# Kernel optimization log

Measured on AMD Instinct MI355X. Metric: run time of the kernel, lower is better.

Reference implementation:

```python
import jax, jax.numpy as jnp
import numpy as np
import math

B, T, EMB, HD = 4, 2048, 2048, 128
HALF = HD // 2


def setup_inputs() -> dict:
    key = jax.random.key(0)
    ks = jax.random.split(key, 4)
    x = jax.random.normal(ks[0], (B, T, EMB), dtype=jnp.float32)
    s = 1.0 / math.sqrt(EMB)
    Wq = jax.random.normal(ks[1], (EMB, HD), dtype=jnp.float32) * s
    Wk = jax.random.normal(ks[2], (EMB, HD), dtype=jnp.float32) * s
    Wv = jax.random.normal(ks[3], (EMB, HD), dtype=jnp.float32) * s
    # Standard RoPE rotation table: theta_i = 10000^(-2i/HD), angle = pos * theta
    inv_freq = 1.0 / (10000.0 ** (np.arange(0, HALF, dtype=np.float32) / HALF))
    angles = np.arange(T, dtype=np.float32)[:, None] * inv_freq[None, :]  # [T, HALF]
    rot_cos = jnp.asarray(np.cos(angles), dtype=jnp.float32)
    rot_sin = jnp.asarray(np.sin(angles), dtype=jnp.float32)
    # Additive causal mask: 0 on/below diagonal, -1e9 above
    NEG = -1e9
    mask = jnp.where(jnp.tril(jnp.ones((T, T), dtype=bool)), 0.0, NEG).astype(jnp.float32)
    return {"x": x, "Wq": Wq, "Wk": Wk, "Wv": Wv,
            "rot_cos": rot_cos, "rot_sin": rot_sin, "mask": mask}


def _apply_rope(q, rot_cos, rot_sin):
    # q: [B, T, HD]; view last dim as HALF complex pairs and rotate
    qp = q.reshape(q.shape[0], q.shape[1], HALF, 2)
    re, im = qp[..., 0], qp[..., 1]
    out_re = re * rot_cos - im * rot_sin  # broadcast [T,HALF] over batch
    out_im = re * rot_sin + im * rot_cos
    return jnp.stack([out_re, out_im], axis=-1).reshape(q.shape)


def reference(x, Wq, Wk, Wv, rot_cos, rot_sin, mask):
    Q = x @ Wq  # [B, T, HD]
    K = x @ Wk
    V = x @ Wv
    Q = _apply_rope(Q, rot_cos, rot_sin)
    K = _apply_rope(K, rot_cos, rot_sin)
    scores = jnp.einsum('bqd,bkd->bqk', Q, K) / math.sqrt(HD)
    probs = jax.nn.softmax(scores + mask, axis=-1)  # dropout is identity in eval
    return jnp.einsum('bqk,bkd->bqd', probs, V)
```

## Files before the change

kernel.cpp:

```cpp
#include <hip/hip_runtime.h>
#include <cstddef>
#include <cstdint>

#define T_SEQ 2048
#define EMB_D 2048
#define HD_D  128

typedef __attribute__((ext_vector_type(8))) short short8;
typedef __attribute__((ext_vector_type(4))) float f32x4;
typedef __attribute__((ext_vector_type(4))) unsigned short ushort4v;
typedef __attribute__((ext_vector_type(8))) unsigned short ushort8v;

union frag_u { short8 s8; unsigned u[4]; };

static __device__ __forceinline__ unsigned short f2bf_rne(float f) {
    union { float f; unsigned u; } v; v.f = f;
    unsigned r = v.u + 0x7fffu + ((v.u >> 16) & 1u);
    return (unsigned short)(r >> 16);
}
static __device__ __forceinline__ unsigned short f2bf_fast(float f) {
    union { float f; unsigned u; } v; v.f = f;
    return (unsigned short)((v.u + 0x8000u) >> 16);
}
static __device__ __forceinline__ unsigned pk2(float a, float b) {
    union { float f; unsigned u; } x, y; x.f = a; y.f = b;
    return __builtin_amdgcn_perm(y.u + 0x8000u, x.u + 0x8000u, 0x07060302);
}
static __device__ __forceinline__ void dma16(const void* g, void* l) {
    __builtin_amdgcn_global_load_lds(
        (const __attribute__((address_space(1))) unsigned int*)g,
        (__attribute__((address_space(3))) unsigned int*)l, 16, 0, 0);
}
#define EXP2F(x) __builtin_amdgcn_exp2f(x)

__global__ __launch_bounds__(256) void prep_weights(
    const float* __restrict__ Wq, const float* __restrict__ Wk,
    const float* __restrict__ Wv, unsigned short* __restrict__ Wt)
{
    __shared__ __attribute__((aligned(16))) unsigned short tw[64 * 132];
    const int w = blockIdx.y;
    const int k0 = blockIdx.x * 64;
    const float* W = (w == 0) ? Wq : (w == 1) ? Wk : Wv;
    const int tid = threadIdx.x;
#pragma unroll
    for (int p = 0; p < 8; p++) {
        const int f = p * 256 + tid;
        const int row = f >> 5, c4 = f & 31;
        const float4 v = *(const float4*)&W[(size_t)(k0 + row) * HD_D + c4 * 4];
        ushort4v h = { f2bf_rne(v.x), f2bf_rne(v.y), f2bf_rne(v.z), f2bf_rne(v.w) };
        *(ushort4v*)&tw[row * 132 + c4 * 4] = h;
    }
    __syncthreads();
    const int n = tid >> 1, h = tid & 1;
    unsigned short* dst = Wt + (size_t)w * (HD_D * EMB_D) + (size_t)n * EMB_D + k0 + h * 32;
#pragma unroll
    for (int j = 0; j < 4; j++) {
        ushort8v o;
#pragma unroll
        for (int jj = 0; jj < 8; jj++) o[jj] = tw[(h * 32 + j * 8 + jj) * 132 + n];
        *(ushort8v*)&dst[j * 8] = o;
    }
}

__global__ __launch_bounds__(256, 2) void qkv_fused(
    const float* __restrict__ x, const unsigned short* __restrict__ Wt,
    const float* __restrict__ rcos, const float* __restrict__ rsin,
    unsigned short* __restrict__ Qb, unsigned short* __restrict__ Kb,
    unsigned short* __restrict__ Vt)
{
    __shared__ __attribute__((aligned(16))) float xs[2][64 * 64];
    __shared__ __attribute__((aligned(16))) unsigned short wsb[2][96 * 64];
    const int ng = blockIdx.x;
    const int m0 = blockIdx.y * 64;
    const int tid = threadIdx.x;
    const int lane = tid & 63, wave = tid >> 6;
    const int wm = wave >> 1, wn = wave & 1;
    const int l15 = lane & 15, lq = lane >> 4;

    const float* xSrc[4]; int xOff[4];
#pragma unroll
    for (int p = 0; p < 4; p++) {
        const int g = p * 256 + tid;
        const int row = g >> 4, c = g & 15;
        xSrc[p] = x + (size_t)(m0 + row) * EMB_D + (c ^ (row & 15)) * 4;
        xOff[p] = (p * 256 + wave * 64) * 4;
    }
    const unsigned short* wSrc[3]; int wOff[3];
#pragma unroll
    for (int p = 0; p < 3; p++) {
        const int g = p * 256 + tid;
        const int row = g >> 3, c = g & 7;
        wSrc[p] = Wt + (size_t)(ng * 96 + row) * EMB_D + (c ^ (row & 7)) * 8;
        wOff[p] = (p * 256 + wave * 64) * 8;
    }

    int offA[2][2][2];
#pragma unroll
    for (int i = 0; i < 2; i++)
#pragma unroll
        for (int ks = 0; ks < 2; ks++) {
            const int row = wm * 32 + i * 16 + l15;
            const int ga = ks * 8 + lq * 2;
            offA[i][ks][0] = row * 64 + ((ga)     ^ (row & 15)) * 4;
            offA[i][ks][1] = row * 64 + ((ga + 1) ^ (row & 15)) * 4;
        }
    int offB[3][2];
#pragma unroll
    for (int j = 0; j < 3; j++)
#pragma unroll
        for (int ks = 0; ks < 2; ks++) {
            const int row = wn * 48 + j * 16 + l15;
            const int gb = ks * 4 + lq;
            offB[j][ks] = row * 64 + (gb ^ (row & 7)) * 8;
        }

    f32x4 acc[2][3];
#pragma unroll
    for (int i = 0; i < 2; i++)
#pragma unroll
        for (int j = 0; j < 3; j++) acc[i][j] = (f32x4){0.f, 0.f, 0.f, 0.f};

#pragma unroll
    for (int p = 0; p < 4; p++) dma16(xSrc[p], &xs[0][xOff[p]]);
#pragma unroll
    for (int p = 0; p < 3; p++) dma16(wSrc[p], &wsb[0][wOff[p]]);

    for (int k0 = 0; k0 < EMB_D; k0 += 64) {
        const int buf = (k0 >> 6) & 1;
        __syncthreads();
        if (k0 + 64 < EMB_D) {
#pragma unroll
            for (int p = 0; p < 4; p++)
                dma16(xSrc[p] + k0 + 64, &xs[buf ^ 1][xOff[p]]);
#pragma unroll
            for (int p = 0; p < 3; p++)
                dma16(wSrc[p] + k0 + 64, &wsb[buf ^ 1][wOff[p]]);
        }

        frag_u A[2][2];
#pragma unroll
        for (int i = 0; i < 2; i++)
#pragma unroll
            for (int ks = 0; ks < 2; ks++) {
                const f32x4 f0 = *(const f32x4*)&xs[buf][offA[i][ks][0]];
                const f32x4 f1 = *(const f32x4*)&xs[buf][offA[i][ks][1]];
                A[i][ks].u[0] = pk2(f0.x, f0.y);
                A[i][ks].u[1] = pk2(f0.z, f0.w);
                A[i][ks].u[2] = pk2(f1.x, f1.y);
                A[i][ks].u[3] = pk2(f1.z, f1.w);
            }
#pragma unroll
        for (int ks = 0; ks < 2; ks++)
#pragma unroll
            for (int j = 0; j < 3; j++) {
                const short8 B = *(const short8*)&wsb[buf][offB[j][ks]];
#pragma unroll
                for (int i = 0; i < 2; i++)
                    acc[i][j] = __builtin_amdgcn_mfma_f32_16x16x32_bf16(
                        A[i][ks].s8, B, acc[i][j], 0, 0, 0);
            }
    }

    const float qscale = 0.08838834764831845f * 1.4426950408889634f;
#pragma unroll
    for (int i = 0; i < 2; i++) {
#pragma unroll
        for (int r = 0; r < 4; r++) {
            const int row = m0 + wm * 32 + i * 16 + lq * 4 + r;
            const int t = row & (T_SEQ - 1);
            const int bb = row >> 11;
#pragma unroll
            for (int j = 0; j < 3; j++) {
                const int col = ng * 96 + wn * 48 + j * 16 + l15;
                const int mat = col >> 7, mcol = col & 127;
                const float v = acc[i][j][r];
                if (mat == 2) {
                    Vt[((size_t)bb * HD_D + mcol) * T_SEQ + t] = f2bf_rne(v);
                } else {
                    const int ip = mcol >> 1;
                    const float c = rcos[t * 64 + ip];
                    const float s = rsin[t * 64 + ip];
                    const float pv = __shfl_xor(v, 1);
                    float rv = (mcol & 1) ? (pv * s + v * c) : (v * c - pv * s);
                    if (mat == 0) {
                        rv *= qscale;
                        Qb[(size_t)row * HD_D + mcol] = f2bf_rne(rv);
                    } else {
                        Kb[(size_t)row * HD_D + mcol] = f2bf_rne(rv);
                    }
                }
            }
        }
    }
}

__global__ __launch_bounds__(256, 2) void attn(
    const unsigned short* __restrict__ Qb, const unsigned short* __restrict__ Kb,
    const unsigned short* __restrict__ Vt, float* __restrict__ out)
{
    __shared__ float O_s[4][16 * 128];
    __shared__ __attribute__((aligned(16))) unsigned short P_s[4][2][16 * 40];
    __shared__ float l_s[4][16];

    const int tid = threadIdx.x;
    const int lane = tid & 63, wave = tid >> 6;
    const int l15 = lane & 15, lq = lane >> 4;
    const int kf = lq * 8;

    const int b  = blockIdx.x & 3;
    const int q0 = (127 - (blockIdx.x >> 2)) * 16;
    const int kend = q0 + 16;
    const float M2 = 16.0f;

    const unsigned short* Qp = Qb + (size_t)(b * T_SEQ + q0) * HD_D;
    short8 aQ[4];
#pragma unroll
    for (int d = 0; d < 4; d++)
        aQ[d] = *(const short8*)&Qp[l15 * HD_D + d * 32 + kf];

    f32x4 acc[8];
#pragma unroll
    for (int d = 0; d < 8; d++) acc[d] = (f32x4){0.f, 0.f, 0.f, 0.f};
    float l_r[4] = {0.f, 0.f, 0.f, 0.f};

    const unsigned short* Kbase = Kb + (size_t)b * T_SEQ * HD_D;
    const unsigned short* Vbase = Vt + (size_t)b * HD_D * T_SEQ;
    unsigned short* PwA = &P_s[wave][0][0];
    unsigned short* PwB = &P_s[wave][1][0];

    for (int c = wave; c * 32 < kend; c += 8) {
        const int kA = c * 32;
        const int kB = (c + 4) * 32;
        const bool hB = kB < kend;

        const unsigned short* KpA = Kbase + (size_t)kA * HD_D;
        const unsigned short* KpB = Kbase + (size_t)kB * HD_D;
        short8 KA[8], KB_[8];
#pragma unroll
        for (int d = 0; d < 4; d++)
#pragma unroll
            for (int n = 0; n < 2; n++)
                KA[d * 2 + n] = *(const short8*)&KpA[(size_t)(n * 16 + l15) * HD_D + d * 32 + kf];
        if (hB) {
#pragma unroll
            for (int d = 0; d < 4; d++)
#pragma unroll
                for (int n = 0; n < 2; n++)
                    KB_[d * 2 + n] = *(const short8*)&KpB[(size_t)(n * 16 + l15) * HD_D + d * 32 + kf];
        }

        f32x4 sA0 = (f32x4){0.f, 0.f, 0.f, 0.f}, sA1 = sA0, sB0 = sA0, sB1 = sA0;
#pragma unroll
        for (int d = 0; d < 4; d++) {
            sA0 = __builtin_amdgcn_mfma_f32_16x16x32_bf16(aQ[d], KA[d * 2 + 0], sA0, 0, 0, 0);
            sA1 = __builtin_amdgcn_mfma_f32_16x16x32_bf16(aQ[d], KA[d * 2 + 1], sA1, 0, 0, 0);
        }
        if (hB) {
#pragma unroll
            for (int d = 0; d < 4; d++) {
                sB0 = __builtin_amdgcn_mfma_f32_16x16x32_bf16(aQ[d], KB_[d * 2 + 0], sB0, 0, 0, 0);
                sB1 = __builtin_amdgcn_mfma_f32_16x16x32_bf16(aQ[d], KB_[d * 2 + 1], sB1, 0, 0, 0);
            }
        }

        short8 VA[8];
#pragma unroll
        for (int d = 0; d < 8; d++)
            VA[d] = *(const short8*)&Vbase[(size_t)(d * 16 + l15) * T_SEQ + kA + kf];

#pragma unroll
        for (int r = 0; r < 4; r++) {
            const int q = q0 + lq * 4 + r;
            const float p0 = ((kA + l15)      <= q) ? EXP2F(sA0[r] - M2) : 0.f;
            const float p1 = ((kA + 16 + l15) <= q) ? EXP2F(sA1[r] - M2) : 0.f;
            l_r[r] += p0 + p1;
            const int prow = (lq * 4 + r) * 40;
            PwA[prow + l15]      = f2bf_fast(p0);
            PwA[prow + 16 + l15] = f2bf_fast(p1);
        }
        const short8 pA = *(const short8*)&PwA[l15 * 40 + kf];
#pragma unroll
        for (int d = 0; d < 8; d++)
            acc[d] = __builtin_amdgcn_mfma_f32_16x16x32_bf16(pA, VA[d], acc[d], 0, 0, 0);

        if (hB) {
            short8 VB[8];
#pragma unroll
            for (int d = 0; d < 8; d++)
                VB[d] = *(const short8*)&Vbase[(size_t)(d * 16 + l15) * T_SEQ + kB + kf];
#pragma unroll
            for (int r = 0; r < 4; r++) {
                const int q = q0 + lq * 4 + r;
                const float p0 = ((kB + l15)      <= q) ? EXP2F(sB0[r] - M2) : 0.f;
                const float p1 = ((kB + 16 + l15) <= q) ? EXP2F(sB1[r] - M2) : 0.f;
                l_r[r] += p0 + p1;
                const int prow = (lq * 4 + r) * 40;
                PwB[prow + l15]      = f2bf_fast(p0);
                PwB[prow + 16 + l15] = f2bf_fast(p1);
            }
            const short8 pB = *(const short8*)&PwB[l15 * 40 + kf];
#pragma unroll
            for (int d = 0; d < 8; d++)
                acc[d] = __builtin_amdgcn_mfma_f32_16x16x32_bf16(pB, VB[d], acc[d], 0, 0, 0);
        }
    }

#pragma unroll
    for (int r = 0; r < 4; r++) {
        float lr = l_r[r];
        lr += __shfl_xor(lr, 1);
        lr += __shfl_xor(lr, 2);
        lr += __shfl_xor(lr, 4);
        lr += __shfl_xor(lr, 8);
        if (l15 == 0) l_s[wave][lq * 4 + r] = lr;
#pragma unroll
        for (int d = 0; d < 8; d++)
            O_s[wave][(lq * 4 + r) * 128 + d * 16 + l15] = acc[d][r];
    }
    __syncthreads();

    const int row = tid >> 4;
    const int dc = (tid & 15) * 8;
    const float lt = l_s[0][row] + l_s[1][row] + l_s[2][row] + l_s[3][row];
    const float inv = 1.0f / lt;
    f32x4 o0 = (f32x4){0.f, 0.f, 0.f, 0.f};
    f32x4 o1 = (f32x4){0.f, 0.f, 0.f, 0.f};
#pragma unroll
    for (int w2 = 0; w2 < 4; w2++) {
        const float* p = &O_s[w2][row * 128 + dc];
        o0 += *(const f32x4*)p;
        o1 += *(const f32x4*)(p + 4);
    }
    float* op = out + (size_t)(b * T_SEQ + q0 + row) * HD_D + dc;
    *(f32x4*)op       = o0 * inv;
    *(f32x4*)(op + 4) = o1 * inv;
}

extern "C" void kernel_launch(void* const* d_in, const int* in_sizes, int n_in,
                              void* d_out, int out_size, void* d_ws, size_t ws_size,
                              hipStream_t stream)
{
    (void)in_sizes; (void)n_in; (void)out_size; (void)ws_size;
    const float* x  = (const float*)d_in[0];
    const float* Wq = (const float*)d_in[1];
    const float* Wk = (const float*)d_in[2];
    const float* Wv = (const float*)d_in[3];
    const float* rc = (const float*)d_in[4];
    const float* rs = (const float*)d_in[5];
    float* out = (float*)d_out;

    char* ws = (char*)d_ws;
    unsigned short* Wt = (unsigned short*)(ws);
    unsigned short* Qb = (unsigned short*)(ws + 1572864);
    unsigned short* Kb = (unsigned short*)(ws + 1572864 + 2097152);
    unsigned short* Vt = (unsigned short*)(ws + 1572864 + 2 * 2097152);

    prep_weights<<<dim3(32, 3),  256, 0, stream>>>(Wq, Wk, Wv, Wt);
    qkv_fused   <<<dim3(4, 128), 256, 0, stream>>>(x, Wt, rc, rs, Qb, Kb, Vt);
    attn        <<<dim3(512),    256, 0, stream>>>(Qb, Kb, Vt, out);
}
```

Measured before the change: 199.5 us.

## Split attention KV range across two blocks and merge partials; remap QKV blocks per XCD

Each query tile's KV loop is now split across two blocks (g=0/1). Block 0 writes fp32 partial output to out and block 1 writes a bf16 partial to workspace, and a new merge kernel sums the two and divides by the combined row sums. This doubles the attention grid to fill more CUs and raises occupancy to 4 blocks per SM, with the partial-sum staging in LDS cut to bf16. The QKV GEMM grid is flattened and remapped so that consecutive row tiles land on the same XCD for L2 reuse. The cost is an extra kernel launch, an extra pass over the output, and added bf16 rounding error in the partial sums.

```diff
diff --git a/kernel.cpp b/kernel.cpp
--- a/kernel.cpp
+++ b/kernel.cpp
@@ -21,6 +21,10 @@
 static __device__ __forceinline__ unsigned short f2bf_fast(float f) {
     union { float f; unsigned u; } v; v.f = f;
     return (unsigned short)((v.u + 0x8000u) >> 16);
+}
+static __device__ __forceinline__ float bf2f(unsigned short h) {
+    union { unsigned u; float f; } v; v.u = ((unsigned)h) << 16;
+    return v.f;
 }
 static __device__ __forceinline__ unsigned pk2(float a, float b) {
     union { float f; unsigned u; } x, y; x.f = a; y.f = b;
@@ -70,8 +74,10 @@
 {
     __shared__ __attribute__((aligned(16))) float xs[2][64 * 64];
     __shared__ __attribute__((aligned(16))) unsigned short wsb[2][96 * 64];
-    const int ng = blockIdx.x;
-    const int m0 = blockIdx.y * 64;
+    const int L = blockIdx.x;
+    const int xcd = L & 7, s = L >> 3;
+    const int ng = s & 3;
+    const int m0 = (xcd * 16 + (s >> 2)) * 64;
     const int tid = threadIdx.x;
     const int lane = tid & 63, wave = tid >> 6;
     const int wm = wave >> 1, wn = wave & 1;
@@ -179,9 +185,9 @@
                 } else {
                     const int ip = mcol >> 1;
                     const float c = rcos[t * 64 + ip];
-                    const float s = rsin[t * 64 + ip];
+                    const float s2 = rsin[t * 64 + ip];
                     const float pv = __shfl_xor(v, 1);
-                    float rv = (mcol & 1) ? (pv * s + v * c) : (v * c - pv * s);
+                    float rv = (mcol & 1) ? (pv * s2 + v * c) : (v * c - pv * s2);
                     if (mat == 0) {
                         rv *= qscale;
                         Qb[(size_t)row * HD_D + mcol] = f2bf_rne(rv);
@@ -194,11 +200,12 @@
     }
 }
 
-__global__ __launch_bounds__(256, 2) void attn(
+__global__ __launch_bounds__(256, 4) void attn(
     const unsigned short* __restrict__ Qb, const unsigned short* __restrict__ Kb,
-    const unsigned short* __restrict__ Vt, float* __restrict__ out)
-{
-    __shared__ float O_s[4][16 * 128];
+    const unsigned short* __restrict__ Vt, float* __restrict__ O0,
+    unsigned short* __restrict__ O1, float* __restrict__ Lp)
+{
+    __shared__ __attribute__((aligned(16))) unsigned short O_s[4][16 * 128];
     __shared__ __attribute__((aligned(16))) unsigned short P_s[4][2][16 * 40];
     __shared__ float l_s[4][16];
 
@@ -207,8 +214,10 @@
     const int l15 = lane & 15, lq = lane >> 4;
     const int kf = lq * 8;
 
-    const int b  = blockIdx.x & 3;
-    const int q0 = (127 - (blockIdx.x >> 2)) * 16;
+    const int L = blockIdx.x;
+    const int g = L & 1;
+    const int b = (L >> 1) & 3;
+    const int q0 = (127 - (L >> 3)) * 16;
     const int kend = q0 + 16;
     const float M2 = 16.0f;
 
@@ -228,9 +237,9 @@
     unsigned short* PwA = &P_s[wave][0][0];
     unsigned short* PwB = &P_s[wave][1][0];
 
-    for (int c = wave; c * 32 < kend; c += 8) {
+    for (int c = 2 * wave + g; c * 32 < kend; c += 16) {
         const int kA = c * 32;
-        const int kB = (c + 4) * 32;
+        const int kB = (c + 8) * 32;
         const bool hB = kB < kend;
 
         const unsigned short* KpA = Kbase + (size_t)kA * HD_D;
@@ -315,25 +324,47 @@
         if (l15 == 0) l_s[wave][lq * 4 + r] = lr;
 #pragma unroll
         for (int d = 0; d < 8; d++)
-            O_s[wave][(lq * 4 + r) * 128 + d * 16 + l15] = acc[d][r];
+            O_s[wave][(lq * 4 + r) * 128 + d * 16 + l15] = f2bf_fast(acc[d][r]);
     }
     __syncthreads();
 
     const int row = tid >> 4;
     const int dc = (tid & 15) * 8;
     const float lt = l_s[0][row] + l_s[1][row] + l_s[2][row] + l_s[3][row];
-    const float inv = 1.0f / lt;
-    f32x4 o0 = (f32x4){0.f, 0.f, 0.f, 0.f};
-    f32x4 o1 = (f32x4){0.f, 0.f, 0.f, 0.f};
+    float o[8];
+#pragma unroll
+    for (int k = 0; k < 8; k++) o[k] = 0.f;
 #pragma unroll
     for (int w2 = 0; w2 < 4; w2++) {
-        const float* p = &O_s[w2][row * 128 + dc];
-        o0 += *(const f32x4*)p;
-        o1 += *(const f32x4*)(p + 4);
-    }
-    float* op = out + (size_t)(b * T_SEQ + q0 + row) * HD_D + dc;
-    *(f32x4*)op       = o0 * inv;
-    *(f32x4*)(op + 4) = o1 * inv;
+        const ushort8v pv = *(const ushort8v*)&O_s[w2][row * 128 + dc];
+#pragma unroll
+        for (int k = 0; k < 8; k++) o[k] += bf2f(pv[k]);
+    }
+    const size_t grow = (size_t)(b * T_SEQ + q0 + row);
+    if (g == 0) {
+        float* op = O0 + grow * HD_D + dc;
+#pragma unroll
+        for (int k = 0; k < 8; k++) op[k] = o[k];
+    } else {
+        ushort8v h;
+#pragma unroll
+        for (int k = 0; k < 8; k++) h[k] = f2bf_fast(o[k]);
+        *(ushort8v*)&O1[grow * HD_D + dc] = h;
+    }
+    if ((tid & 15) == 0) Lp[g * 8192 + grow] = lt;
+}
+
+__global__ __launch_bounds__(256) void attn_merge(
+    float* __restrict__ out, const unsigned short* __restrict__ O1,
+    const float* __restrict__ Lp)
+{
+    const int idx = blockIdx.x * 256 + threadIdx.x;
+    const int row = idx >> 5;
+    f32x4 a = ((f32x4*)out)[idx];
+    const ushort4v h = ((const ushort4v*)O1)[idx];
+    f32x4 bv = { bf2f(h.x), bf2f(h.y), bf2f(h.z), bf2f(h.w) };
+    const float inv = 1.0f / (Lp[row] + Lp[8192 + row]);
+    ((f32x4*)out)[idx] = (a + bv) * inv;
 }
 
 extern "C" void kernel_launch(void* const* d_in, const int* in_sizes, int n_in,
@@ -352,10 +383,13 @@
     char* ws = (char*)d_ws;
     unsigned short* Wt = (unsigned short*)(ws);
     unsigned short* Qb = (unsigned short*)(ws + 1572864);
-    unsigned short* Kb = (unsigned short*)(ws + 1572864 + 2097152);
-    unsigned short* Vt = (unsigned short*)(ws + 1572864 + 2 * 2097152);
-
-    prep_weights<<<dim3(32, 3),  256, 0, stream>>>(Wq, Wk, Wv, Wt);
-    qkv_fused   <<<dim3(4, 128), 256, 0, stream>>>(x, Wt, rc, rs, Qb, Kb, Vt);
-    attn        <<<dim3(512),    256, 0, stream>>>(Qb, Kb, Vt, out);
-}
+    unsigned short* Kb = (unsigned short*)(ws + 3670016);
+    unsigned short* Vt = (unsigned short*)(ws + 5767168);
+    unsigned short* O1 = (unsigned short*)(ws + 7864320);
+    float*          Lp = (float*)(ws + 9961472);
+
+    prep_weights<<<dim3(32, 3), 256, 0, stream>>>(Wq, Wk, Wv, Wt);
+    qkv_fused   <<<dim3(512),   256, 0, stream>>>(x, Wt, rc, rs, Qb, Kb, Vt);
+    attn        <<<dim3(1024),  256, 0, stream>>>(Qb, Kb, Vt, out, O1, Lp);
+    attn_merge  <<<dim3(1024),  256, 0, stream>>>(out, O1, Lp);
+}
```

Result: slower. 229.3 us (+14.9%).
